# Optimization experiments

Hardware: AMD Instinct MI355X
Metric: run time of the kernel (lower is better)

## Reference

```python
import jax, jax.numpy as jnp
import numpy as np

D = H = W = 128  # voxel grid resolution (shape = [1,1,128,128,128] in source)
N = 2_000_000    # number of points


def splat(vals, pts, d, h, w):
    """Adjoint of trilinear F.grid_sample (align_corners=False, zeros padding).
    vals: [N] point values; pts: [N,3] normalized (x,y,z) coords in [-1,1].
    Returns [d,h,w] voxel grid with trilinear scatter-add of vals.
    """
    # unnormalize: pixel = ((coord+1)*size - 1) / 2  (align_corners=False)
    x = ((pts[:, 0] + 1.0) * w - 1.0) * 0.5
    y = ((pts[:, 1] + 1.0) * h - 1.0) * 0.5
    z = ((pts[:, 2] + 1.0) * d - 1.0) * 0.5
    x0 = jnp.floor(x); y0 = jnp.floor(y); z0 = jnp.floor(z)
    fx = x - x0; fy = y - y0; fz = z - z0
    x0i = x0.astype(jnp.int32); y0i = y0.astype(jnp.int32); z0i = z0.astype(jnp.int32)
    grid = jnp.zeros((d * h * w,), dtype=vals.dtype)
    for dz in (0, 1):
        wz = fz if dz else (1.0 - fz)
        for dy in (0, 1):
            wy = fy if dy else (1.0 - fy)
            for dx in (0, 1):
                wx = fx if dx else (1.0 - fx)
                xi = x0i + dx; yi = y0i + dy; zi = z0i + dz
                valid = (xi >= 0) & (xi < w) & (yi >= 0) & (yi < h) & (zi >= 0) & (zi < d)
                idx = jnp.where(valid, (zi * h + yi) * w + xi, 0)
                contrib = jnp.where(valid, wx * wy * wz * vals, 0.0)
                grid = grid.at[idx].add(contrib)
    return grid.reshape(d, h, w)


def huber_sum(pred, gt, delta=1.0):
    diff = pred - gt
    a = jnp.abs(diff)
    return jnp.sum(jnp.where(a <= delta, 0.5 * diff * diff, delta * (a - 0.5 * delta)))


def setup_inputs() -> dict:
    key = jax.random.key(0)
    k1, k2, k3 = jax.random.split(key, 3)
    coords = jax.random.uniform(k1, (1, N, 3), jnp.float32, -0.95, 0.95)
    registration_pred = 0.02 * jax.random.normal(k2, (1, N, 3), jnp.float32)
    registration_gt = 0.02 * jax.random.normal(k3, (1, N, 3), jnp.float32)
    return {"registration_pred": registration_pred,
            "registration_gt": registration_gt,
            "coords": coords}


def reference(registration_pred, registration_gt, coords):
    pred_pts = (coords + registration_pred).reshape(-1, 3)   # [N,3]
    gt_pts = (coords + registration_gt).reshape(-1, 3)       # [N,3]
    vals = jnp.ones((pred_pts.shape[0],), dtype=coords.dtype)
    pred_rast = splat(vals, pred_pts, D, H, W)   # [128,128,128]
    gt_rast = splat(vals, gt_pts, D, H, W)       # [128,128,128]
    return huber_sum(pred_rast, gt_rast)
```

## Files before the change

### kernel.cpp

```cpp
#include <hip/hip_runtime.h>
#include <stdint.h>

constexpr int GRID_R = 128;
constexpr int NVOX = GRID_R * GRID_R * GRID_R;

constexpr int TILE = 16;
constexpr int TPD = GRID_R / TILE;
constexpr int NBINS = TPD * TPD * TPD;
constexpr int CAP = 13312;
constexpr int CUR_STRIDE = 16;
constexpr size_t CUR_BYTES = (size_t)NBINS * CUR_STRIDE * sizeof(uint32_t);
constexpr size_t ITEMS_BYTES = (size_t)NBINS * CAP * sizeof(uint2);
constexpr size_t SORT_WS_NEEDED = CUR_BYTES + ITEMS_BYTES;

constexpr uint32_t SENT_W1 = 0xFFFFFFFFu;

constexpr int PAD = 18;

constexpr int QXB = 9;
constexpr int QZSTRIDE = QXB * QXB;
constexpr int QARR = PAD * QZSTRIDE;
constexpr float QSCALE = 1024.0f;

__device__ __forceinline__ int axis_tiles(int c0, int* ts, int* ls) {
    int n = 0;
    if ((unsigned)c0 < (unsigned)GRID_R) {
        int tx = c0 >> 4; ts[0] = tx; ls[0] = c0 - (tx << 4); n = 1;
    }
    int c1 = c0 + 1;
    if ((unsigned)c1 < (unsigned)GRID_R) {
        int tx = c1 >> 4;
        if (!n || tx != ts[0]) { ts[n] = tx; ls[n] = c0 - (tx << 4); ++n; }
    }
    return n;
}

template <typename F>
__device__ __forceinline__ void for_each_replica(float px, float py, float pz,
                                                 uint32_t g, F&& emit) {
    float x0f = floorf(px), y0f = floorf(py), z0f = floorf(pz);
    int x0 = (int)x0f, y0 = (int)y0f, z0 = (int)z0f;
    float fx = px - x0f, fy = py - y0f, fz = pz - z0f;

    int txs[2], lxs[2], tys[2], lys[2], tzs[2], lzs[2];
    int ntx = axis_tiles(x0, txs, lxs);
    int nty = axis_tiles(y0, tys, lys);
    int ntz = axis_tiles(z0, tzs, lzs);
    if (!ntx || !nty || !ntz) return;

    uint32_t ufx = (uint32_t)(fx * 65535.0f + 0.5f);
    uint32_t ufy = (uint32_t)(fy * 65535.0f + 0.5f);
    uint32_t ufz = (uint32_t)(fz * 65535.0f + 0.5f);
    uint32_t w0 = ufx | (ufy << 16);

    for (int c = 0; c < ntz; ++c)
        for (int b = 0; b < nty; ++b)
            for (int a = 0; a < ntx; ++a) {
                int bin = (tzs[c] * TPD + tys[b]) * TPD + txs[a];
                uint32_t w1 = ufz |
                              ((uint32_t)(lxs[a] + 1) << 16) |
                              ((uint32_t)(lys[b] + 1) << 21) |
                              ((uint32_t)(lzs[c] + 1) << 26) |
                              (g << 31);
                emit(bin, w0, w1);
            }
}

__device__ __forceinline__ void load_pts(const float* __restrict__ pred_reg,
                                         const float* __restrict__ gt_reg,
                                         const float* __restrict__ coords,
                                         int i, float* pa, float* pb) {
    float cx = coords[3 * i + 0], cy = coords[3 * i + 1], cz = coords[3 * i + 2];
    pa[0] = (cx + pred_reg[3 * i + 0] + 1.0f) * 64.0f - 0.5f;
    pa[1] = (cy + pred_reg[3 * i + 1] + 1.0f) * 64.0f - 0.5f;
    pa[2] = (cz + pred_reg[3 * i + 2] + 1.0f) * 64.0f - 0.5f;
    pb[0] = (cx + gt_reg[3 * i + 0] + 1.0f) * 64.0f - 0.5f;
    pb[1] = (cy + gt_reg[3 * i + 1] + 1.0f) * 64.0f - 0.5f;
    pb[2] = (cz + gt_reg[3 * i + 2] + 1.0f) * 64.0f - 0.5f;
}

#define SBLOCK 1024
#define PPT 4
constexpr int RCAP = 16;

__global__ __launch_bounds__(SBLOCK) void scatter_kernel(
        const float* __restrict__ pred_reg, const float* __restrict__ gt_reg,
        const float* __restrict__ coords, uint32_t* __restrict__ cursors,
        uint2* __restrict__ items, int n) {
    __shared__ alignas(16) uint2 ring[NBINS * RCAP];
    __shared__ uint32_t pc[NBINS];
    __shared__ uint32_t fl[NBINS];
    int t = threadIdx.x;
    if (t < NBINS) { pc[t] = 0; fl[t] = 0; }
    __syncthreads();

    int i0 = blockIdx.x * (SBLOCK * PPT);

    for (int k = 0; k < PPT; ++k) {
        int i = i0 + k * SBLOCK + t;
        if (i < n) {
            float pa[3], pb[3];
            load_pts(pred_reg, gt_reg, coords, i, pa, pb);
            auto emit = [&](int bin, uint32_t w0, uint32_t w1) {
                uint32_t base = fl[bin] * 8u;
                uint32_t r = atomicAdd(&pc[bin], 1u);
                if (r - base < (uint32_t)RCAP) {
                    ring[bin * RCAP + (int)(r & (RCAP - 1))] = make_uint2(w0, w1);
                } else {
                    atomicSub(&pc[bin], 1u);
                    uint32_t s = atomicAdd(&cursors[bin * CUR_STRIDE], 1u);
                    if (s < (uint32_t)CAP)
                        items[(size_t)bin * CAP + s] = make_uint2(w0, w1);
                }
            };
            for_each_replica(pa[0], pa[1], pa[2], 0u, emit);
            for_each_replica(pb[0], pb[1], pb[2], 1u, emit);
        }
        __syncthreads();
        if (t < NBINS) {
            uint32_t f = fl[t], p = pc[t];
            uint32_t ng = (p - f * 8u) >> 3;
            if (ng) {
                uint32_t s0 = atomicAdd(&cursors[t * CUR_STRIDE], ng * 8u);
                for (uint32_t g = 0; g < ng; ++g) {
                    uint32_t sb = s0 + g * 8u;
                    int rb = t * RCAP + (int)(((f + g) & 1u) << 3);
                    uint2* dst = items + (size_t)t * CAP + sb;
                    if (sb + 8u <= (uint32_t)CAP) {
#pragma unroll
                        for (int j = 0; j < 8; ++j) dst[j] = ring[rb + j];
                    } else {
                        for (int j = 0; j < 8; ++j)
                            if (sb + j < (uint32_t)CAP) dst[j] = ring[rb + j];
                    }
                }
                fl[t] = f + ng;
            }
        }
        __syncthreads();
    }

    if (t < NBINS) {
        uint32_t f = fl[t], p = pc[t];
        uint32_t fb = f * 8u;
        uint32_t res = p - fb;
        if (res) {
            uint32_t r2 = (res + 1u) & ~1u;
            for (uint32_t j = res; j < r2; ++j)
                ring[t * RCAP + (int)((fb + j) & (RCAP - 1))] =
                    make_uint2(0u, SENT_W1);
            uint32_t s0 = atomicAdd(&cursors[t * CUR_STRIDE], r2);
            for (uint32_t j = 0; j < r2; ++j) {
                uint32_t s = s0 + j;
                if (s < (uint32_t)CAP)
                    items[(size_t)t * CAP + s] =
                        ring[t * RCAP + (int)((fb + j) & (RCAP - 1))];
            }
        }
    }
}

#define ABLOCK 1024

__device__ __forceinline__ void accum_item(uint64_t* __restrict__ U,
                                           uint32_t wx, uint32_t wy) {
    int lx1 = (int)((wy >> 16) & 31u);
    if (lx1 == 31) return;
    float fx = (float)(wx & 0xffffu) * (1.0f / 65535.0f);
    float fy = (float)(wx >> 16) * (1.0f / 65535.0f);
    float fz = (float)(wy & 0xffffu) * (1.0f / 65535.0f);
    int ly1 = (int)((wy >> 21) & 31u);
    int lz1 = (int)((wy >> 26) & 31u);
    uint32_t g = wy >> 31;

    int px = lx1 & 1, xb = lx1 >> 1;
    int py = ly1 & 1, yb = ly1 >> 1;
    uint64_t* arr = U + ((g << 2) | (py << 1) | px) * QARR;
    int idx = lz1 * QZSTRIDE + yb * QXB + xb;

    float wx1 = fx, wx0 = 1.0f - fx;
    float wy1 = fy, wy0 = 1.0f - fy;
    float q00 = wx0 * wy0 * QSCALE, q10 = wx1 * wy0 * QSCALE;
    float q01 = wx0 * wy1 * QSCALE, q11 = wx1 * wy1 * QSCALE;
    float wz1 = fz, wz0 = 1.0f - fz;

    auto pk = [&](float wz) -> uint64_t {
        uint32_t lo = (uint32_t)(q00 * wz + 0.5f) |
                      ((uint32_t)(q10 * wz + 0.5f) << 16);
        uint32_t hi = (uint32_t)(q01 * wz + 0.5f) |
                      ((uint32_t)(q11 * wz + 0.5f) << 16);
        return (uint64_t)lo | ((uint64_t)hi << 32);
    };
    atomicAdd((unsigned long long*)&arr[idx],
              (unsigned long long)pk(wz0));
    atomicAdd((unsigned long long*)&arr[idx + QZSTRIDE],
              (unsigned long long)pk(wz1));
}

__global__ __launch_bounds__(ABLOCK, 4) void accum_kernel(
        const uint2* __restrict__ items, const uint32_t* __restrict__ cursors,
        float* __restrict__ out) {
    __shared__ uint64_t U[8 * QARR];
    __shared__ float wsum[ABLOCK / 64];
    int bin = blockIdx.x, t = threadIdx.x;

    for (int j = t; j < 8 * QARR; j += ABLOCK) U[j] = 0ull;
    __syncthreads();

    uint32_t cnt = cursors[bin * CUR_STRIDE];
    if (cnt > (uint32_t)CAP) cnt = CAP;
    const uint2* seg = items + (size_t)bin * CAP;
    const uint4* seg4 = (const uint4*)seg;
    uint32_t npair = cnt >> 1;

    uint32_t i = t;
    uint4 w = (i < npair) ? seg4[i] : make_uint4(0, 0, 0, 0);
    while (i < npair) {
        uint32_t inext = i + ABLOCK;
        uint4 wn = (inext < npair) ? seg4[inext] : make_uint4(0, 0, 0, 0);
        accum_item(U, w.x, w.y);
        accum_item(U, w.z, w.w);
        w = wn; i = inext;
    }
    if ((cnt & 1) && t == 0) {
        uint2 lw = seg[cnt - 1];
        accum_item(U, lw.x, lw.y);
    }
    __syncthreads();

    float s = 0.0f;
    for (int j = t; j < TILE * TILE * TILE; j += ABLOCK) {
        int x = (j & 15) + 1, y = ((j >> 4) & 15) + 1, z = (j >> 8) + 1;
        float v[2];
#pragma unroll
        for (int g = 0; g < 2; ++g) {
            float acc = 0.0f;
#pragma unroll
            for (int py = 0; py < 2; ++py)
#pragma unroll
                for (int px = 0; px < 2; ++px) {
                    int xb = (x - px) >> 1, lx = (x - px) & 1;
                    int yb = (y - py) >> 1, ly = (y - py) & 1;
                    uint64_t q = U[((g << 2) | (py << 1) | px) * QARR +
                                   z * QZSTRIDE + yb * QXB + xb];
                    acc += (float)((uint32_t)(q >> (((ly << 1) | lx) << 4)) &
                                   0xFFFFu);
                }
            v[g] = acc;
        }
        float d = (v[0] - v[1]) * (1.0f / QSCALE);
        float aa = fabsf(d);
        s += (aa <= 1.0f) ? 0.5f * d * d : (aa - 0.5f);
    }
#pragma unroll
    for (int off = 32; off > 0; off >>= 1) s += __shfl_down(s, off, 64);
    int lane = t & 63, wid = t >> 6;
    if (!lane) wsum[wid] = s;
    __syncthreads();
    if (!t) {
        float tot = 0.0f;
#pragma unroll
        for (int wv = 0; wv < ABLOCK / 64; ++wv) tot += wsum[wv];
        unsafeAtomicAdd(out, tot);
    }
}

__device__ __forceinline__ void splat_point(float nx, float ny, float nz,
                                            float* __restrict__ grid) {
    float x = (nx + 1.0f) * 64.0f - 0.5f;
    float y = (ny + 1.0f) * 64.0f - 0.5f;
    float z = (nz + 1.0f) * 64.0f - 0.5f;
    float x0f = floorf(x), y0f = floorf(y), z0f = floorf(z);
    float fx = x - x0f, fy = y - y0f, fz = z - z0f;
    int x0 = (int)x0f, y0 = (int)y0f, z0 = (int)z0f;
    int xs[2] = {x0, x0 + 1}, ys[2] = {y0, y0 + 1}, zs[2] = {z0, z0 + 1};
    float wxs[2] = {1.0f - fx, fx}, wys[2] = {1.0f - fy, fy}, wzs[2] = {1.0f - fz, fz};
#pragma unroll
    for (int dz = 0; dz < 2; ++dz) {
        int zi = zs[dz]; if ((unsigned)zi >= (unsigned)GRID_R) continue;
#pragma unroll
        for (int dy = 0; dy < 2; ++dy) {
            int yi = ys[dy]; if ((unsigned)yi >= (unsigned)GRID_R) continue;
            float wzy = wzs[dz] * wys[dy];
            int basei = (zi * GRID_R + yi) * GRID_R;
#pragma unroll
            for (int dx = 0; dx < 2; ++dx) {
                int xi = xs[dx]; if ((unsigned)xi >= (unsigned)GRID_R) continue;
                unsafeAtomicAdd(&grid[basei + xi], wzy * wxs[dx]);
            }
        }
    }
}

__global__ void splat_kernel(const float* __restrict__ pred_reg,
                             const float* __restrict__ gt_reg,
                             const float* __restrict__ coords,
                             float* __restrict__ gridA, float* __restrict__ gridB,
                             int n) {
    int i = blockIdx.x * blockDim.x + threadIdx.x;
    if (i >= n) return;
    float cx = coords[3 * i + 0], cy = coords[3 * i + 1], cz = coords[3 * i + 2];
    splat_point(cx + pred_reg[3 * i + 0], cy + pred_reg[3 * i + 1],
                cz + pred_reg[3 * i + 2], gridA);
    splat_point(cx + gt_reg[3 * i + 0], cy + gt_reg[3 * i + 1],
                cz + gt_reg[3 * i + 2], gridB);
}

__global__ void huber_kernel(const float4* __restrict__ A,
                             const float4* __restrict__ B,
                             float* __restrict__ out) {
    int i = blockIdx.x * blockDim.x + threadIdx.x;
    float4 a = A[i], b = B[i];
    auto h1 = [](float d) { float x = fabsf(d);
                            return (x <= 1.0f) ? 0.5f * d * d : (x - 0.5f); };
    float s = h1(a.x - b.x) + h1(a.y - b.y) + h1(a.z - b.z) + h1(a.w - b.w);
#pragma unroll
    for (int off = 32; off > 0; off >>= 1) s += __shfl_down(s, off, 64);
    __shared__ float wsum[4];
    int lane = threadIdx.x & 63, wid = threadIdx.x >> 6;
    if (!lane) wsum[wid] = s;
    __syncthreads();
    if (!threadIdx.x) atomicAdd(out, wsum[0] + wsum[1] + wsum[2] + wsum[3]);
}

extern "C" void kernel_launch(void* const* d_in, const int* in_sizes, int n_in,
                              void* d_out, int out_size, void* d_ws, size_t ws_size,
                              hipStream_t stream) {
    const float* pred_reg = (const float*)d_in[0];
    const float* gt_reg   = (const float*)d_in[1];
    const float* coords   = (const float*)d_in[2];
    float* outp = (float*)d_out;
    int n = in_sizes[2] / 3;

    hipMemsetAsync(d_out, 0, sizeof(float), stream);

    if (ws_size >= SORT_WS_NEEDED) {
        uint32_t* cursors = (uint32_t*)d_ws;
        uint2* items = (uint2*)((char*)d_ws + CUR_BYTES);
        hipMemsetAsync(cursors, 0, CUR_BYTES, stream);

        int sblocks = (n + SBLOCK * PPT - 1) / (SBLOCK * PPT);
        scatter_kernel<<<sblocks, SBLOCK, 0, stream>>>(pred_reg, gt_reg, coords,
                                                       cursors, items, n);
        accum_kernel<<<NBINS, ABLOCK, 0, stream>>>(items, cursors, outp);
    } else {
        float* gridA = (float*)d_ws;
        float* gridB = gridA + NVOX;
        hipMemsetAsync(d_ws, 0, (size_t)2 * NVOX * sizeof(float), stream);
        int blocks = (n + 255) / 256;
        splat_kernel<<<blocks, 256, 0, stream>>>(pred_reg, gt_reg, coords,
                                                 gridA, gridB, n);
        huber_kernel<<<NVOX / 4 / 256, 256, 0, stream>>>((const float4*)gridA,
                                                         (const float4*)gridB, outp);
    }
}
```

Measured before the change: 160.2 us.

## Fuse scatter and accumulate stages into one cooperative kernel with grid syncs

Replaces the two memsets, the scatter kernel and the accumulate kernel with a single cooperative launch of 256 blocks of 1024 threads. Each block zeroes part of the cursors and the output, binning runs with eight points per thread, and after a grid-wide sync each block accumulates two bins in sequence. The ring buffer reuses the shared accumulator array, so both phases fit in one LDS allocation. This removes launch and memset overhead, at the cost of grid.sync latency, fewer blocks in the binning phase, and serialised per-block bin processing that can worsen load imbalance.

After: 238.0 us. 48.5% more time.

```diff
diff --git a/kernel.cpp b/kernel.cpp
--- a/kernel.cpp
+++ b/kernel.cpp
@@ -1,5 +1,8 @@
 #include <hip/hip_runtime.h>
+#include <hip/hip_cooperative_groups.h>
 #include <stdint.h>
+
+namespace cg = cooperative_groups;
 
 constexpr int GRID_R = 128;
 constexpr int NVOX = GRID_R * GRID_R * GRID_R;
@@ -21,6 +24,11 @@
 constexpr int QZSTRIDE = QXB * QXB;
 constexpr int QARR = PAD * QZSTRIDE;
 constexpr float QSCALE = 1024.0f;
+
+constexpr int FBLOCKS = 256;
+constexpr int FTHREADS = 1024;
+#define PPT 8
+constexpr int RCAP = 16;
 
 __device__ __forceinline__ int axis_tiles(int c0, int* ts, int* ls) {
     int n = 0;
@@ -79,89 +87,6 @@
     pb[2] = (cz + gt_reg[3 * i + 2] + 1.0f) * 64.0f - 0.5f;
 }
 
-#define SBLOCK 1024
-#define PPT 4
-constexpr int RCAP = 16;
-
-__global__ __launch_bounds__(SBLOCK) void scatter_kernel(
-        const float* __restrict__ pred_reg, const float* __restrict__ gt_reg,
-        const float* __restrict__ coords, uint32_t* __restrict__ cursors,
-        uint2* __restrict__ items, int n) {
-    __shared__ alignas(16) uint2 ring[NBINS * RCAP];
-    __shared__ uint32_t pc[NBINS];
-    __shared__ uint32_t fl[NBINS];
-    int t = threadIdx.x;
-    if (t < NBINS) { pc[t] = 0; fl[t] = 0; }
-    __syncthreads();
-
-    int i0 = blockIdx.x * (SBLOCK * PPT);
-
-    for (int k = 0; k < PPT; ++k) {
-        int i = i0 + k * SBLOCK + t;
-        if (i < n) {
-            float pa[3], pb[3];
-            load_pts(pred_reg, gt_reg, coords, i, pa, pb);
-            auto emit = [&](int bin, uint32_t w0, uint32_t w1) {
-                uint32_t base = fl[bin] * 8u;
-                uint32_t r = atomicAdd(&pc[bin], 1u);
-                if (r - base < (uint32_t)RCAP) {
-                    ring[bin * RCAP + (int)(r & (RCAP - 1))] = make_uint2(w0, w1);
-                } else {
-                    atomicSub(&pc[bin], 1u);
-                    uint32_t s = atomicAdd(&cursors[bin * CUR_STRIDE], 1u);
-                    if (s < (uint32_t)CAP)
-                        items[(size_t)bin * CAP + s] = make_uint2(w0, w1);
-                }
-            };
-            for_each_replica(pa[0], pa[1], pa[2], 0u, emit);
-            for_each_replica(pb[0], pb[1], pb[2], 1u, emit);
-        }
-        __syncthreads();
-        if (t < NBINS) {
-            uint32_t f = fl[t], p = pc[t];
-            uint32_t ng = (p - f * 8u) >> 3;
-            if (ng) {
-                uint32_t s0 = atomicAdd(&cursors[t * CUR_STRIDE], ng * 8u);
-                for (uint32_t g = 0; g < ng; ++g) {
-                    uint32_t sb = s0 + g * 8u;
-                    int rb = t * RCAP + (int)(((f + g) & 1u) << 3);
-                    uint2* dst = items + (size_t)t * CAP + sb;
-                    if (sb + 8u <= (uint32_t)CAP) {
-#pragma unroll
-                        for (int j = 0; j < 8; ++j) dst[j] = ring[rb + j];
-                    } else {
-                        for (int j = 0; j < 8; ++j)
-                            if (sb + j < (uint32_t)CAP) dst[j] = ring[rb + j];
-                    }
-                }
-                fl[t] = f + ng;
-            }
-        }
-        __syncthreads();
-    }
-
-    if (t < NBINS) {
-        uint32_t f = fl[t], p = pc[t];
-        uint32_t fb = f * 8u;
-        uint32_t res = p - fb;
-        if (res) {
-            uint32_t r2 = (res + 1u) & ~1u;
-            for (uint32_t j = res; j < r2; ++j)
-                ring[t * RCAP + (int)((fb + j) & (RCAP - 1))] =
-                    make_uint2(0u, SENT_W1);
-            uint32_t s0 = atomicAdd(&cursors[t * CUR_STRIDE], r2);
-            for (uint32_t j = 0; j < r2; ++j) {
-                uint32_t s = s0 + j;
-                if (s < (uint32_t)CAP)
-                    items[(size_t)t * CAP + s] =
-                        ring[t * RCAP + (int)((fb + j) & (RCAP - 1))];
-            }
-        }
-    }
-}
-
-#define ABLOCK 1024
-
 __device__ __forceinline__ void accum_item(uint64_t* __restrict__ U,
                                            uint32_t wx, uint32_t wy) {
     int lx1 = (int)((wy >> 16) & 31u);
@@ -197,71 +122,158 @@
               (unsigned long long)pk(wz1));
 }
 
-__global__ __launch_bounds__(ABLOCK, 4) void accum_kernel(
-        const uint2* __restrict__ items, const uint32_t* __restrict__ cursors,
-        float* __restrict__ out) {
-    __shared__ uint64_t U[8 * QARR];
-    __shared__ float wsum[ABLOCK / 64];
-    int bin = blockIdx.x, t = threadIdx.x;
-
-    for (int j = t; j < 8 * QARR; j += ABLOCK) U[j] = 0ull;
-    __syncthreads();
-
-    uint32_t cnt = cursors[bin * CUR_STRIDE];
-    if (cnt > (uint32_t)CAP) cnt = CAP;
-    const uint2* seg = items + (size_t)bin * CAP;
-    const uint4* seg4 = (const uint4*)seg;
-    uint32_t npair = cnt >> 1;
-
-    uint32_t i = t;
-    uint4 w = (i < npair) ? seg4[i] : make_uint4(0, 0, 0, 0);
-    while (i < npair) {
-        uint32_t inext = i + ABLOCK;
-        uint4 wn = (inext < npair) ? seg4[inext] : make_uint4(0, 0, 0, 0);
-        accum_item(U, w.x, w.y);
-        accum_item(U, w.z, w.w);
-        w = wn; i = inext;
-    }
-    if ((cnt & 1) && t == 0) {
-        uint2 lw = seg[cnt - 1];
-        accum_item(U, lw.x, lw.y);
-    }
-    __syncthreads();
-
-    float s = 0.0f;
-    for (int j = t; j < TILE * TILE * TILE; j += ABLOCK) {
-        int x = (j & 15) + 1, y = ((j >> 4) & 15) + 1, z = (j >> 8) + 1;
-        float v[2];
-#pragma unroll
-        for (int g = 0; g < 2; ++g) {
-            float acc = 0.0f;
-#pragma unroll
-            for (int py = 0; py < 2; ++py)
-#pragma unroll
-                for (int px = 0; px < 2; ++px) {
-                    int xb = (x - px) >> 1, lx = (x - px) & 1;
-                    int yb = (y - py) >> 1, ly = (y - py) & 1;
-                    uint64_t q = U[((g << 2) | (py << 1) | px) * QARR +
-                                   z * QZSTRIDE + yb * QXB + xb];
-                    acc += (float)((uint32_t)(q >> (((ly << 1) | lx) << 4)) &
-                                   0xFFFFu);
+__global__ __launch_bounds__(FTHREADS) void fused_kernel(
+        const float* __restrict__ pred_reg, const float* __restrict__ gt_reg,
+        const float* __restrict__ coords, uint32_t* __restrict__ cursors,
+        uint2* __restrict__ items, float* __restrict__ out, int n) {
+    cg::grid_group grid = cg::this_grid();
+    __shared__ alignas(16) uint64_t U[8 * QARR];
+    __shared__ float wsum[FTHREADS / 64];
+    int t = threadIdx.x, b = blockIdx.x;
+
+    {
+        int j = b * FTHREADS + t;
+        if (j < NBINS * CUR_STRIDE) cursors[j] = 0;
+        if (j == 0) *out = 0.0f;
+    }
+    grid.sync();
+
+    {
+        uint2* ring = reinterpret_cast<uint2*>(U);
+        uint32_t* pc = reinterpret_cast<uint32_t*>(U + 8192);
+        uint32_t* fl = pc + NBINS;
+        if (t < NBINS) { pc[t] = 0; fl[t] = 0; }
+        __syncthreads();
+
+        int i0 = b * (FTHREADS * PPT);
+        for (int k = 0; k < PPT; ++k) {
+            int i = i0 + k * FTHREADS + t;
+            if (i < n) {
+                float pa[3], pb[3];
+                load_pts(pred_reg, gt_reg, coords, i, pa, pb);
+                auto emit = [&](int bin, uint32_t w0, uint32_t w1) {
+                    uint32_t base = fl[bin] * 8u;
+                    uint32_t r = atomicAdd(&pc[bin], 1u);
+                    if (r - base < (uint32_t)RCAP) {
+                        ring[bin * RCAP + (int)(r & (RCAP - 1))] =
+                            make_uint2(w0, w1);
+                    } else {
+                        atomicSub(&pc[bin], 1u);
+                        uint32_t s = atomicAdd(&cursors[bin * CUR_STRIDE], 1u);
+                        if (s < (uint32_t)CAP)
+                            items[(size_t)bin * CAP + s] = make_uint2(w0, w1);
+                    }
+                };
+                for_each_replica(pa[0], pa[1], pa[2], 0u, emit);
+                for_each_replica(pb[0], pb[1], pb[2], 1u, emit);
+            }
+            __syncthreads();
+            if (t < NBINS) {
+                uint32_t f = fl[t], p = pc[t];
+                uint32_t ng = (p - f * 8u) >> 3;
+                if (ng) {
+                    uint32_t s0 = atomicAdd(&cursors[t * CUR_STRIDE], ng * 8u);
+                    for (uint32_t g = 0; g < ng; ++g) {
+                        uint32_t sb = s0 + g * 8u;
+                        int rb = t * RCAP + (int)(((f + g) & 1u) << 3);
+                        uint2* dst = items + (size_t)t * CAP + sb;
+                        if (sb + 8u <= (uint32_t)CAP) {
+#pragma unroll
+                            for (int j = 0; j < 8; ++j) dst[j] = ring[rb + j];
+                        } else {
+                            for (int j = 0; j < 8; ++j)
+                                if (sb + j < (uint32_t)CAP) dst[j] = ring[rb + j];
+                        }
+                    }
+                    fl[t] = f + ng;
                 }
-            v[g] = acc;
-        }
-        float d = (v[0] - v[1]) * (1.0f / QSCALE);
-        float aa = fabsf(d);
-        s += (aa <= 1.0f) ? 0.5f * d * d : (aa - 0.5f);
-    }
-#pragma unroll
-    for (int off = 32; off > 0; off >>= 1) s += __shfl_down(s, off, 64);
-    int lane = t & 63, wid = t >> 6;
-    if (!lane) wsum[wid] = s;
-    __syncthreads();
-    if (!t) {
-        float tot = 0.0f;
-#pragma unroll
-        for (int wv = 0; wv < ABLOCK / 64; ++wv) tot += wsum[wv];
-        unsafeAtomicAdd(out, tot);
+            }
+            __syncthreads();
+        }
+
+        if (t < NBINS) {
+            uint32_t f = fl[t], p = pc[t];
+            uint32_t fb = f * 8u;
+            uint32_t res = p - fb;
+            if (res) {
+                uint32_t r2 = (res + 1u) & ~1u;
+                for (uint32_t j = res; j < r2; ++j)
+                    ring[t * RCAP + (int)((fb + j) & (RCAP - 1))] =
+                        make_uint2(0u, SENT_W1);
+                uint32_t s0 = atomicAdd(&cursors[t * CUR_STRIDE], r2);
+                for (uint32_t j = 0; j < r2; ++j) {
+                    uint32_t s = s0 + j;
+                    if (s < (uint32_t)CAP)
+                        items[(size_t)t * CAP + s] =
+                            ring[t * RCAP + (int)((fb + j) & (RCAP - 1))];
+                }
+            }
+        }
+    }
+    grid.sync();
+
+    for (int pass = 0; pass < 2; ++pass) {
+        int bin = b * 2 + pass;
+        __syncthreads();
+        for (int j = t; j < 8 * QARR; j += FTHREADS) U[j] = 0ull;
+        __syncthreads();
+
+        uint32_t cnt = cursors[bin * CUR_STRIDE];
+        if (cnt > (uint32_t)CAP) cnt = CAP;
+        const uint2* seg = items + (size_t)bin * CAP;
+        const uint4* seg4 = (const uint4*)seg;
+        uint32_t npair = cnt >> 1;
+
+        uint32_t i = t;
+        uint4 w = (i < npair) ? seg4[i] : make_uint4(0, 0, 0, 0);
+        while (i < npair) {
+            uint32_t inext = i + FTHREADS;
+            uint4 wn = (inext < npair) ? seg4[inext] : make_uint4(0, 0, 0, 0);
+            accum_item(U, w.x, w.y);
+            accum_item(U, w.z, w.w);
+            w = wn; i = inext;
+        }
+        if ((cnt & 1) && t == 0) {
+            uint2 lw = seg[cnt - 1];
+            accum_item(U, lw.x, lw.y);
+        }
+        __syncthreads();
+
+        float s = 0.0f;
+        for (int j = t; j < TILE * TILE * TILE; j += FTHREADS) {
+            int x = (j & 15) + 1, y = ((j >> 4) & 15) + 1, z = (j >> 8) + 1;
+            float v[2];
+#pragma unroll
+            for (int g = 0; g < 2; ++g) {
+                float acc = 0.0f;
+#pragma unroll
+                for (int py = 0; py < 2; ++py)
+#pragma unroll
+                    for (int px = 0; px < 2; ++px) {
+                        int xb = (x - px) >> 1, lx = (x - px) & 1;
+                        int yb = (y - py) >> 1, ly = (y - py) & 1;
+                        uint64_t q = U[((g << 2) | (py << 1) | px) * QARR +
+                                       z * QZSTRIDE + yb * QXB + xb];
+                        acc += (float)((uint32_t)(q >> (((ly << 1) | lx) << 4)) &
+                                       0xFFFFu);
+                    }
+                v[g] = acc;
+            }
+            float d = (v[0] - v[1]) * (1.0f / QSCALE);
+            float aa = fabsf(d);
+            s += (aa <= 1.0f) ? 0.5f * d * d : (aa - 0.5f);
+        }
+#pragma unroll
+        for (int off = 32; off > 0; off >>= 1) s += __shfl_down(s, off, 64);
+        int lane = t & 63, wid = t >> 6;
+        if (!lane) wsum[wid] = s;
+        __syncthreads();
+        if (!t) {
+            float tot = 0.0f;
+#pragma unroll
+            for (int wv = 0; wv < FTHREADS / 64; ++wv) tot += wsum[wv];
+            unsafeAtomicAdd(out, tot);
+        }
     }
 }
 
@@ -332,18 +344,16 @@
     float* outp = (float*)d_out;
     int n = in_sizes[2] / 3;
 
-    hipMemsetAsync(d_out, 0, sizeof(float), stream);
-
     if (ws_size >= SORT_WS_NEEDED) {
         uint32_t* cursors = (uint32_t*)d_ws;
         uint2* items = (uint2*)((char*)d_ws + CUR_BYTES);
-        hipMemsetAsync(cursors, 0, CUR_BYTES, stream);
-
-        int sblocks = (n + SBLOCK * PPT - 1) / (SBLOCK * PPT);
-        scatter_kernel<<<sblocks, SBLOCK, 0, stream>>>(pred_reg, gt_reg, coords,
-                                                       cursors, items, n);
-        accum_kernel<<<NBINS, ABLOCK, 0, stream>>>(items, cursors, outp);
+        void* args[] = {(void*)&pred_reg, (void*)&gt_reg, (void*)&coords,
+                        (void*)&cursors, (void*)&items, (void*)&outp, (void*)&n};
+        hipLaunchCooperativeKernel((const void*)fused_kernel,
+                                   dim3(FBLOCKS), dim3(FTHREADS),
+                                   args, 0, stream);
     } else {
+        hipMemsetAsync(d_out, 0, sizeof(float), stream);
         float* gridA = (float*)d_ws;
         float* gridB = gridA + NVOX;
         hipMemsetAsync(d_ws, 0, (size_t)2 * NVOX * sizeof(float), stream);
```

## Split each bin's accumulation across two z-half blocks and vectorize ring flushes

Applied to the files above, without the earlier changes.

Each spatial bin is now handled by two accumulation blocks, each owning half the z range, so there are twice as many blocks and each uses a smaller shared-memory array. Every block still reads the full item list and discards items outside its z half. The scatter kernel now writes ring flushes as uint4 stores and pads single overflow items with a sentinel to keep stores 16-byte aligned. The output memset is folded into the scatter kernel to drop one launch. The cost is duplicated item reads in the accumulation phase, and the padded overflow writes use more buffer capacity.

Measured after the change: 162.9 us. About the same (+1.7%).

```diff
diff --git a/kernel.cpp b/kernel.cpp
--- a/kernel.cpp
+++ b/kernel.cpp
@@ -19,7 +19,7 @@
 
 constexpr int QXB = 9;
 constexpr int QZSTRIDE = QXB * QXB;
-constexpr int QARR = PAD * QZSTRIDE;
+constexpr int QARR_H = 10 * QZSTRIDE;
 constexpr float QSCALE = 1024.0f;
 
 __device__ __forceinline__ int axis_tiles(int c0, int* ts, int* ls) {
@@ -86,12 +86,13 @@
 __global__ __launch_bounds__(SBLOCK) void scatter_kernel(
         const float* __restrict__ pred_reg, const float* __restrict__ gt_reg,
         const float* __restrict__ coords, uint32_t* __restrict__ cursors,
-        uint2* __restrict__ items, int n) {
+        uint2* __restrict__ items, float* __restrict__ out, int n) {
     __shared__ alignas(16) uint2 ring[NBINS * RCAP];
     __shared__ uint32_t pc[NBINS];
     __shared__ uint32_t fl[NBINS];
     int t = threadIdx.x;
     if (t < NBINS) { pc[t] = 0; fl[t] = 0; }
+    if (blockIdx.x == 0 && t == 0) *out = 0.0f;
     __syncthreads();
 
     int i0 = blockIdx.x * (SBLOCK * PPT);
@@ -108,9 +109,11 @@
                     ring[bin * RCAP + (int)(r & (RCAP - 1))] = make_uint2(w0, w1);
                 } else {
                     atomicSub(&pc[bin], 1u);
-                    uint32_t s = atomicAdd(&cursors[bin * CUR_STRIDE], 1u);
-                    if (s < (uint32_t)CAP)
-                        items[(size_t)bin * CAP + s] = make_uint2(w0, w1);
+                    uint32_t s = atomicAdd(&cursors[bin * CUR_STRIDE], 2u);
+                    if (s + 2u <= (uint32_t)CAP) {
+                        uint4* dst = (uint4*)(items + (size_t)bin * CAP + s);
+                        *dst = make_uint4(w0, w1, 0u, SENT_W1);
+                    }
                 }
             };
             for_each_replica(pa[0], pa[1], pa[2], 0u, emit);
@@ -122,16 +125,19 @@
             uint32_t ng = (p - f * 8u) >> 3;
             if (ng) {
                 uint32_t s0 = atomicAdd(&cursors[t * CUR_STRIDE], ng * 8u);
+                const uint4* rsrc = (const uint4*)&ring[t * RCAP];
                 for (uint32_t g = 0; g < ng; ++g) {
                     uint32_t sb = s0 + g * 8u;
-                    int rb = t * RCAP + (int)(((f + g) & 1u) << 3);
-                    uint2* dst = items + (size_t)t * CAP + sb;
+                    const uint4* src = rsrc + ((int)((f + g) & 1u)) * 4;
                     if (sb + 8u <= (uint32_t)CAP) {
-#pragma unroll
-                        for (int j = 0; j < 8; ++j) dst[j] = ring[rb + j];
+                        uint4* dst = (uint4*)(items + (size_t)t * CAP + sb);
+                        dst[0] = src[0]; dst[1] = src[1];
+                        dst[2] = src[2]; dst[3] = src[3];
                     } else {
+                        int rb = t * RCAP + (int)(((f + g) & 1u) << 3);
                         for (int j = 0; j < 8; ++j)
-                            if (sb + j < (uint32_t)CAP) dst[j] = ring[rb + j];
+                            if (sb + j < (uint32_t)CAP)
+                                items[(size_t)t * CAP + sb + j] = ring[rb + j];
                     }
                 }
                 fl[t] = f + ng;
@@ -162,21 +168,23 @@
 
 #define ABLOCK 1024
 
-__device__ __forceinline__ void accum_item(uint64_t* __restrict__ U,
-                                           uint32_t wx, uint32_t wy) {
+__device__ __forceinline__ void accum_item_z(uint64_t* __restrict__ U,
+                                             uint32_t wx, uint32_t wy,
+                                             uint32_t zbase) {
+    uint32_t lz1 = (wy >> 26) & 31u;
+    uint32_t rel = lz1 - zbase;
+    if (rel > 8u) return;
     int lx1 = (int)((wy >> 16) & 31u);
-    if (lx1 == 31) return;
+    int ly1 = (int)((wy >> 21) & 31u);
+    uint32_t g = wy >> 31;
     float fx = (float)(wx & 0xffffu) * (1.0f / 65535.0f);
     float fy = (float)(wx >> 16) * (1.0f / 65535.0f);
     float fz = (float)(wy & 0xffffu) * (1.0f / 65535.0f);
-    int ly1 = (int)((wy >> 21) & 31u);
-    int lz1 = (int)((wy >> 26) & 31u);
-    uint32_t g = wy >> 31;
 
     int px = lx1 & 1, xb = lx1 >> 1;
     int py = ly1 & 1, yb = ly1 >> 1;
-    uint64_t* arr = U + ((g << 2) | (py << 1) | px) * QARR;
-    int idx = lz1 * QZSTRIDE + yb * QXB + xb;
+    uint64_t* arr = U + ((g << 2) | (py << 1) | px) * QARR_H;
+    int idx = (int)rel * QZSTRIDE + yb * QXB + xb;
 
     float wx1 = fx, wx0 = 1.0f - fx;
     float wy1 = fy, wy0 = 1.0f - fy;
@@ -197,14 +205,15 @@
               (unsigned long long)pk(wz1));
 }
 
-__global__ __launch_bounds__(ABLOCK, 4) void accum_kernel(
+__global__ __launch_bounds__(ABLOCK) void accum_kernel(
         const uint2* __restrict__ items, const uint32_t* __restrict__ cursors,
         float* __restrict__ out) {
-    __shared__ uint64_t U[8 * QARR];
+    __shared__ uint64_t U[8 * QARR_H];
     __shared__ float wsum[ABLOCK / 64];
-    int bin = blockIdx.x, t = threadIdx.x;
-
-    for (int j = t; j < 8 * QARR; j += ABLOCK) U[j] = 0ull;
+    int bin = blockIdx.x >> 1, t = threadIdx.x;
+    uint32_t zbase = (blockIdx.x & 1) ? 8u : 0u;
+
+    for (int j = t; j < 8 * QARR_H; j += ABLOCK) U[j] = 0ull;
     __syncthreads();
 
     uint32_t cnt = cursors[bin * CUR_STRIDE];
@@ -218,19 +227,19 @@
     while (i < npair) {
         uint32_t inext = i + ABLOCK;
         uint4 wn = (inext < npair) ? seg4[inext] : make_uint4(0, 0, 0, 0);
-        accum_item(U, w.x, w.y);
-        accum_item(U, w.z, w.w);
+        accum_item_z(U, w.x, w.y, zbase);
+        accum_item_z(U, w.z, w.w, zbase);
         w = wn; i = inext;
     }
     if ((cnt & 1) && t == 0) {
         uint2 lw = seg[cnt - 1];
-        accum_item(U, lw.x, lw.y);
+        accum_item_z(U, lw.x, lw.y, zbase);
     }
     __syncthreads();
 
     float s = 0.0f;
-    for (int j = t; j < TILE * TILE * TILE; j += ABLOCK) {
-        int x = (j & 15) + 1, y = ((j >> 4) & 15) + 1, z = (j >> 8) + 1;
+    for (int j = t; j < TILE * TILE * 8; j += ABLOCK) {
+        int x = (j & 15) + 1, y = ((j >> 4) & 15) + 1, zl = (j >> 8) + 1;
         float v[2];
 #pragma unroll
         for (int g = 0; g < 2; ++g) {
@@ -241,8 +250,8 @@
                 for (int px = 0; px < 2; ++px) {
                     int xb = (x - px) >> 1, lx = (x - px) & 1;
                     int yb = (y - py) >> 1, ly = (y - py) & 1;
-                    uint64_t q = U[((g << 2) | (py << 1) | px) * QARR +
-                                   z * QZSTRIDE + yb * QXB + xb];
+                    uint64_t q = U[((g << 2) | (py << 1) | px) * QARR_H +
+                                   zl * QZSTRIDE + yb * QXB + xb];
                     acc += (float)((uint32_t)(q >> (((ly << 1) | lx) << 4)) &
                                    0xFFFFu);
                 }
@@ -332,8 +341,6 @@
     float* outp = (float*)d_out;
     int n = in_sizes[2] / 3;
 
-    hipMemsetAsync(d_out, 0, sizeof(float), stream);
-
     if (ws_size >= SORT_WS_NEEDED) {
         uint32_t* cursors = (uint32_t*)d_ws;
         uint2* items = (uint2*)((char*)d_ws + CUR_BYTES);
@@ -341,9 +348,10 @@
 
         int sblocks = (n + SBLOCK * PPT - 1) / (SBLOCK * PPT);
         scatter_kernel<<<sblocks, SBLOCK, 0, stream>>>(pred_reg, gt_reg, coords,
-                                                       cursors, items, n);
-        accum_kernel<<<NBINS, ABLOCK, 0, stream>>>(items, cursors, outp);
+                                                       cursors, items, outp, n);
+        accum_kernel<<<NBINS * 2, ABLOCK, 0, stream>>>(items, cursors, outp);
     } else {
+        hipMemsetAsync(d_out, 0, sizeof(float), stream);
         float* gridA = (float*)d_ws;
         float* gridB = gridA + NVOX;
         hipMemsetAsync(d_ws, 0, (size_t)2 * NVOX * sizeof(float), stream);
```

## Split bins to 16x16x8 tiles, shrink rings, fold output zeroing into scatter

Applied to the files above, without the earlier changes.

Bins become 1024 tiles of 16x16x8 voxels in place of 512 cubes of 16, so each accumulate block holds a smaller shared-memory halo array and more blocks run the accumulate pass. The per-bin shared ring drops to 8 entries and flushes one 8-item group per round. Overflow writes become 16-byte pairs padded with a sentinel, and the accum occupancy hint is removed. Zeroing of the output moves into the scatter kernel, dropping a memset launch. The trade-off is more z-boundary replicas per point and extra sentinel padding in the item lists.

Measured after the change: 186.0 us. +16.1%, slower.

```diff
diff --git a/kernel.cpp b/kernel.cpp
--- a/kernel.cpp
+++ b/kernel.cpp
@@ -4,10 +4,8 @@
 constexpr int GRID_R = 128;
 constexpr int NVOX = GRID_R * GRID_R * GRID_R;
 
-constexpr int TILE = 16;
-constexpr int TPD = GRID_R / TILE;
-constexpr int NBINS = TPD * TPD * TPD;
-constexpr int CAP = 13312;
+constexpr int NBINS = 1024;
+constexpr int CAP = 6640;
 constexpr int CUR_STRIDE = 16;
 constexpr size_t CUR_BYTES = (size_t)NBINS * CUR_STRIDE * sizeof(uint32_t);
 constexpr size_t ITEMS_BYTES = (size_t)NBINS * CAP * sizeof(uint2);
@@ -15,22 +13,21 @@
 
 constexpr uint32_t SENT_W1 = 0xFFFFFFFFu;
 
-constexpr int PAD = 18;
-
 constexpr int QXB = 9;
 constexpr int QZSTRIDE = QXB * QXB;
-constexpr int QARR = PAD * QZSTRIDE;
+constexpr int ZP = 10;
+constexpr int QARR = ZP * QZSTRIDE;
 constexpr float QSCALE = 1024.0f;
 
-__device__ __forceinline__ int axis_tiles(int c0, int* ts, int* ls) {
+__device__ __forceinline__ int axis_tiles_s(int c0, int* ts, int* ls, int sh) {
     int n = 0;
     if ((unsigned)c0 < (unsigned)GRID_R) {
-        int tx = c0 >> 4; ts[0] = tx; ls[0] = c0 - (tx << 4); n = 1;
+        int tx = c0 >> sh; ts[0] = tx; ls[0] = c0 - (tx << sh); n = 1;
     }
     int c1 = c0 + 1;
     if ((unsigned)c1 < (unsigned)GRID_R) {
-        int tx = c1 >> 4;
-        if (!n || tx != ts[0]) { ts[n] = tx; ls[n] = c0 - (tx << 4); ++n; }
+        int tx = c1 >> sh;
+        if (!n || tx != ts[0]) { ts[n] = tx; ls[n] = c0 - (tx << sh); ++n; }
     }
     return n;
 }
@@ -43,9 +40,9 @@
     float fx = px - x0f, fy = py - y0f, fz = pz - z0f;
 
     int txs[2], lxs[2], tys[2], lys[2], tzs[2], lzs[2];
-    int ntx = axis_tiles(x0, txs, lxs);
-    int nty = axis_tiles(y0, tys, lys);
-    int ntz = axis_tiles(z0, tzs, lzs);
+    int ntx = axis_tiles_s(x0, txs, lxs, 4);
+    int nty = axis_tiles_s(y0, tys, lys, 4);
+    int ntz = axis_tiles_s(z0, tzs, lzs, 3);
     if (!ntx || !nty || !ntz) return;
 
     uint32_t ufx = (uint32_t)(fx * 65535.0f + 0.5f);
@@ -56,7 +53,7 @@
     for (int c = 0; c < ntz; ++c)
         for (int b = 0; b < nty; ++b)
             for (int a = 0; a < ntx; ++a) {
-                int bin = (tzs[c] * TPD + tys[b]) * TPD + txs[a];
+                int bin = (tzs[c] * 8 + tys[b]) * 8 + txs[a];
                 uint32_t w1 = ufz |
                               ((uint32_t)(lxs[a] + 1) << 16) |
                               ((uint32_t)(lys[b] + 1) << 21) |
@@ -81,17 +78,18 @@
 
 #define SBLOCK 1024
 #define PPT 4
-constexpr int RCAP = 16;
+constexpr int RCAP = 8;
 
 __global__ __launch_bounds__(SBLOCK) void scatter_kernel(
         const float* __restrict__ pred_reg, const float* __restrict__ gt_reg,
         const float* __restrict__ coords, uint32_t* __restrict__ cursors,
-        uint2* __restrict__ items, int n) {
+        uint2* __restrict__ items, float* __restrict__ out, int n) {
     __shared__ alignas(16) uint2 ring[NBINS * RCAP];
     __shared__ uint32_t pc[NBINS];
     __shared__ uint32_t fl[NBINS];
     int t = threadIdx.x;
-    if (t < NBINS) { pc[t] = 0; fl[t] = 0; }
+    pc[t] = 0; fl[t] = 0;
+    if (blockIdx.x == 0 && t == 0) *out = 0.0f;
     __syncthreads();
 
     int i0 = blockIdx.x * (SBLOCK * PPT);
@@ -108,39 +106,38 @@
                     ring[bin * RCAP + (int)(r & (RCAP - 1))] = make_uint2(w0, w1);
                 } else {
                     atomicSub(&pc[bin], 1u);
-                    uint32_t s = atomicAdd(&cursors[bin * CUR_STRIDE], 1u);
-                    if (s < (uint32_t)CAP)
-                        items[(size_t)bin * CAP + s] = make_uint2(w0, w1);
+                    uint32_t s = atomicAdd(&cursors[bin * CUR_STRIDE], 2u);
+                    if (s + 2u <= (uint32_t)CAP) {
+                        uint4* dst = (uint4*)(items + (size_t)bin * CAP + s);
+                        *dst = make_uint4(w0, w1, 0u, SENT_W1);
+                    }
                 }
             };
             for_each_replica(pa[0], pa[1], pa[2], 0u, emit);
             for_each_replica(pb[0], pb[1], pb[2], 1u, emit);
         }
         __syncthreads();
-        if (t < NBINS) {
+        {
             uint32_t f = fl[t], p = pc[t];
-            uint32_t ng = (p - f * 8u) >> 3;
-            if (ng) {
-                uint32_t s0 = atomicAdd(&cursors[t * CUR_STRIDE], ng * 8u);
-                for (uint32_t g = 0; g < ng; ++g) {
-                    uint32_t sb = s0 + g * 8u;
-                    int rb = t * RCAP + (int)(((f + g) & 1u) << 3);
-                    uint2* dst = items + (size_t)t * CAP + sb;
-                    if (sb + 8u <= (uint32_t)CAP) {
-#pragma unroll
-                        for (int j = 0; j < 8; ++j) dst[j] = ring[rb + j];
-                    } else {
-                        for (int j = 0; j < 8; ++j)
-                            if (sb + j < (uint32_t)CAP) dst[j] = ring[rb + j];
-                    }
+            if (p - f * 8u >= 8u) {
+                uint32_t s0 = atomicAdd(&cursors[t * CUR_STRIDE], 8u);
+                const uint4* src = (const uint4*)&ring[t * RCAP];
+                if (s0 + 8u <= (uint32_t)CAP) {
+                    uint4* dst = (uint4*)(items + (size_t)t * CAP + s0);
+                    dst[0] = src[0]; dst[1] = src[1];
+                    dst[2] = src[2]; dst[3] = src[3];
+                } else {
+                    for (int j = 0; j < 8; ++j)
+                        if (s0 + j < (uint32_t)CAP)
+                            items[(size_t)t * CAP + s0 + j] = ring[t * RCAP + j];
                 }
-                fl[t] = f + ng;
+                fl[t] = f + 1u;
             }
         }
         __syncthreads();
     }
 
-    if (t < NBINS) {
+    {
         uint32_t f = fl[t], p = pc[t];
         uint32_t fb = f * 8u;
         uint32_t res = p - fb;
@@ -164,19 +161,19 @@
 
 __device__ __forceinline__ void accum_item(uint64_t* __restrict__ U,
                                            uint32_t wx, uint32_t wy) {
+    uint32_t lz1 = (wy >> 26) & 31u;
+    if (lz1 > 9u) return;
     int lx1 = (int)((wy >> 16) & 31u);
-    if (lx1 == 31) return;
+    int ly1 = (int)((wy >> 21) & 31u);
+    uint32_t g = wy >> 31;
     float fx = (float)(wx & 0xffffu) * (1.0f / 65535.0f);
     float fy = (float)(wx >> 16) * (1.0f / 65535.0f);
     float fz = (float)(wy & 0xffffu) * (1.0f / 65535.0f);
-    int ly1 = (int)((wy >> 21) & 31u);
-    int lz1 = (int)((wy >> 26) & 31u);
-    uint32_t g = wy >> 31;
 
     int px = lx1 & 1, xb = lx1 >> 1;
     int py = ly1 & 1, yb = ly1 >> 1;
     uint64_t* arr = U + ((g << 2) | (py << 1) | px) * QARR;
-    int idx = lz1 * QZSTRIDE + yb * QXB + xb;
+    int idx = (int)lz1 * QZSTRIDE + yb * QXB + xb;
 
     float wx1 = fx, wx0 = 1.0f - fx;
     float wy1 = fy, wy0 = 1.0f - fy;
@@ -197,7 +194,7 @@
               (unsigned long long)pk(wz1));
 }
 
-__global__ __launch_bounds__(ABLOCK, 4) void accum_kernel(
+__global__ __launch_bounds__(ABLOCK) void accum_kernel(
         const uint2* __restrict__ items, const uint32_t* __restrict__ cursors,
         float* __restrict__ out) {
     __shared__ uint64_t U[8 * QARR];
@@ -229,8 +226,8 @@
     __syncthreads();
 
     float s = 0.0f;
-    for (int j = t; j < TILE * TILE * TILE; j += ABLOCK) {
-        int x = (j & 15) + 1, y = ((j >> 4) & 15) + 1, z = (j >> 8) + 1;
+    for (int j = t; j < 16 * 16 * 8; j += ABLOCK) {
+        int x = (j & 15) + 1, y = ((j >> 4) & 15) + 1, zl = (j >> 8) + 1;
         float v[2];
 #pragma unroll
         for (int g = 0; g < 2; ++g) {
@@ -242,7 +239,7 @@
                     int xb = (x - px) >> 1, lx = (x - px) & 1;
                     int yb = (y - py) >> 1, ly = (y - py) & 1;
                     uint64_t q = U[((g << 2) | (py << 1) | px) * QARR +
-                                   z * QZSTRIDE + yb * QXB + xb];
+                                   zl * QZSTRIDE + yb * QXB + xb];
                     acc += (float)((uint32_t)(q >> (((ly << 1) | lx) << 4)) &
                                    0xFFFFu);
                 }
@@ -332,8 +329,6 @@
     float* outp = (float*)d_out;
     int n = in_sizes[2] / 3;
 
-    hipMemsetAsync(d_out, 0, sizeof(float), stream);
-
     if (ws_size >= SORT_WS_NEEDED) {
         uint32_t* cursors = (uint32_t*)d_ws;
         uint2* items = (uint2*)((char*)d_ws + CUR_BYTES);
@@ -341,9 +336,10 @@
 
         int sblocks = (n + SBLOCK * PPT - 1) / (SBLOCK * PPT);
         scatter_kernel<<<sblocks, SBLOCK, 0, stream>>>(pred_reg, gt_reg, coords,
-                                                       cursors, items, n);
+                                                       cursors, items, outp, n);
         accum_kernel<<<NBINS, ABLOCK, 0, stream>>>(items, cursors, outp);
     } else {
+        hipMemsetAsync(d_out, 0, sizeof(float), stream);
         float* gridA = (float*)d_ws;
         float* gridB = gridA + NVOX;
         hipMemsetAsync(d_ws, 0, (size_t)2 * NVOX * sizeof(float), stream);
```
